# Kernel optimization log

Measured on AMD Instinct MI355X. Metric: run time of the kernel, lower is better.

The kernel has to match this reference:

```python
import jax, jax.numpy as jnp
import numpy as np

OUT_FEAT = 32  # output_feature; projected dim = OUT_FEAT**2 = 1024
D_K = OUT_FEAT ** 0.5  # NOTE: source divides by sqrt(output_feature), not sqrt(output_feature^2)


def setup_inputs() -> dict:
    key = jax.random.key(0)
    ks = jax.random.split(key, 7)
    N, D_in, D_proj = 4096, 1024, OUT_FEAT * OUT_FEAT
    s = 1.0 / np.sqrt(D_in)
    return {
        "x": jax.random.normal(ks[0], (N, D_in), jnp.float32),
        "Wq": jax.random.normal(ks[1], (D_in, D_proj), jnp.float32) * s,
        "bq": jax.random.normal(ks[2], (D_proj,), jnp.float32) * s,
        "Wk": jax.random.normal(ks[3], (D_in, D_proj), jnp.float32) * s,
        "bk": jax.random.normal(ks[4], (D_proj,), jnp.float32) * s,
        "Wv": jax.random.normal(ks[5], (D_in, D_proj), jnp.float32) * s,
        "bv": jax.random.normal(ks[6], (D_proj,), jnp.float32) * s,
    }


def reference(x, Wq, bq, Wk, bk, Wv, bv):
    # QKV projections: [N, D_proj]
    Q = x @ Wq + bq
    K = x @ Wk + bk
    V = x @ Wv + bv
    # scores: [N, N], scaled by sqrt(output_feature) per the source
    scores = (Q @ K.T) / D_K
    attn_weights = jax.nn.softmax(scores, axis=-1)
    attn_output = attn_weights @ V  # [N, D_proj]
    attn_output = attn_output.reshape(-1, OUT_FEAT, OUT_FEAT)  # mode='cov' reshape
    return attn_output, attn_weights
```

## Files before the change

kernel.cpp:

```cpp
#include <hip/hip_runtime.h>

typedef short short8 __attribute__((ext_vector_type(8)));
typedef float f32x4 __attribute__((ext_vector_type(4)));

constexpr int NROW  = 4096;
constexpr int DIN   = 1024;
constexpr int DPROJ = 1024;
constexpr float INV_DK = 0.17677669529663687f;

__device__ __forceinline__ unsigned short f2bf(float f) {
  union { float f; unsigned int u; } v; v.f = f;
  unsigned int r = v.u + 0x7FFFu + ((v.u >> 16) & 1u);
  return (unsigned short)(r >> 16);
}
__device__ __forceinline__ float bf2f(unsigned short h) {
  union { unsigned int u; float f; } v; v.u = ((unsigned int)h) << 16; return v.f;
}

template<int KB>
__device__ __forceinline__ void stage_tile(const unsigned short* __restrict__ g,
                                           long row0, long ldK, long k0,
                                           unsigned short* lds_tile, int w, int lane) {
  if constexpr (KB == 64) {
    const int rsub = lane >> 3;
    const int csw  = ((lane & 7) ^ (rsub & 7)) * 8;
#pragma unroll
    for (int it = 0; it < 4; ++it) {
      const int rowblk = w * 32 + it * 8;
      const unsigned short* src = g + (row0 + rowblk + rsub) * ldK + k0 + csw;
      unsigned short* dst = lds_tile + rowblk * 64;
      __builtin_amdgcn_global_load_lds(
          (const __attribute__((address_space(1))) unsigned int*)(const void*)src,
          (__attribute__((address_space(3))) unsigned int*)(void*)dst, 16, 0, 0);
    }
  } else {
    const int rsub = lane >> 2;
    const int csw  = ((lane & 3) ^ ((rsub >> 1) & 3)) * 8;
#pragma unroll
    for (int it = 0; it < 2; ++it) {
      const int rowblk = w * 32 + it * 16;
      const unsigned short* src = g + (row0 + rowblk + rsub) * ldK + k0 + csw;
      unsigned short* dst = lds_tile + rowblk * 32;
      __builtin_amdgcn_global_load_lds(
          (const __attribute__((address_space(1))) unsigned int*)(const void*)src,
          (__attribute__((address_space(3))) unsigned int*)(void*)dst, 16, 0, 0);
    }
  }
}

template<int SPLIT, int EPI, int KB>
__global__ __launch_bounds__(256, 2) void mfma_gemm(
    const unsigned short* __restrict__ Ah, const unsigned short* __restrict__ Al,
    const unsigned short* __restrict__ Bh, const unsigned short* __restrict__ Bl,
    const float* __restrict__ bias, float* __restrict__ Cf,
    unsigned short* __restrict__ Coh, unsigned short* __restrict__ Col,
    int M, int N, int K, float alpha)
{
  constexpr int NT = SPLIT ? 4 : 2;
  constexpr int TS = 128 * KB;
  __shared__ __align__(16) unsigned short lds[2][NT * TS];
  const int tid  = threadIdx.x;
  const int w    = tid >> 6, lane = tid & 63;
  const int wr   = w >> 1,   wc   = w & 1;
  const int lrow = lane & 15, lgrp = lane >> 4;
  const long bm = (long)blockIdx.y * 128, bn = (long)blockIdx.x * 128;

  f32x4 acc[4][4] = {};

  const int nsteps = K / KB;

  stage_tile<KB>(Ah, bm, K, 0, &lds[0][0 * TS], w, lane);
  stage_tile<KB>(Bh, bn, K, 0, &lds[0][1 * TS], w, lane);
  if constexpr (SPLIT) {
    stage_tile<KB>(Al, bm, K, 0, &lds[0][2 * TS], w, lane);
    stage_tile<KB>(Bl, bn, K, 0, &lds[0][3 * TS], w, lane);
  }

  int cur = 0;
  for (int t = 0; t < nsteps; ++t) {
    __syncthreads();
    if (t + 1 < nsteps) {
      const long k0 = (long)(t + 1) * KB;
      const int nb = cur ^ 1;
      stage_tile<KB>(Ah, bm, K, k0, &lds[nb][0 * TS], w, lane);
      stage_tile<KB>(Bh, bn, K, k0, &lds[nb][1 * TS], w, lane);
      if constexpr (SPLIT) {
        stage_tile<KB>(Al, bm, K, k0, &lds[nb][2 * TS], w, lane);
        stage_tile<KB>(Bl, bn, K, k0, &lds[nb][3 * TS], w, lane);
      }
    }
    const unsigned short* L = lds[cur];
#pragma unroll
    for (int s = 0; s < KB / 32; ++s) {
      short8 ah[4], bh[4], al[4], bl[4];
#pragma unroll
      for (int i = 0; i < 4; ++i) {
        const int ra  = wr * 64 + i * 16 + lrow;
        const int sga = (KB == 64) ? (ra & 7) : ((ra >> 1) & 3);
        const int cha = ((s * 4 + lgrp) ^ sga);
        const int offa = ra * KB + cha * 8;
        ah[i] = *(const short8*)&L[0 * TS + offa];
        if constexpr (SPLIT) al[i] = *(const short8*)&L[2 * TS + offa];
        const int rb  = wc * 64 + i * 16 + lrow;
        const int sgb = (KB == 64) ? (rb & 7) : ((rb >> 1) & 3);
        const int chb = ((s * 4 + lgrp) ^ sgb);
        const int offb = rb * KB + chb * 8;
        bh[i] = *(const short8*)&L[1 * TS + offb];
        if constexpr (SPLIT) bl[i] = *(const short8*)&L[3 * TS + offb];
      }
#pragma unroll
      for (int i = 0; i < 4; ++i)
#pragma unroll
        for (int j = 0; j < 4; ++j) {
          acc[i][j] = __builtin_amdgcn_mfma_f32_16x16x32_bf16(ah[i], bh[j], acc[i][j], 0, 0, 0);
          if constexpr (SPLIT) {
            acc[i][j] = __builtin_amdgcn_mfma_f32_16x16x32_bf16(ah[i], bl[j], acc[i][j], 0, 0, 0);
            acc[i][j] = __builtin_amdgcn_mfma_f32_16x16x32_bf16(al[i], bh[j], acc[i][j], 0, 0, 0);
          }
        }
    }
    cur ^= 1;
  }

#pragma unroll
  for (int i = 0; i < 4; ++i) {
    const long rbase = bm + wr * 64 + i * 16 + lgrp * 4;
#pragma unroll
    for (int j = 0; j < 4; ++j) {
      const long cg = bn + wc * 64 + j * 16 + lrow;
#pragma unroll
      for (int r = 0; r < 4; ++r) {
        const long rg = rbase + r;
        float v = acc[i][j][r];
        if constexpr (EPI == 0) {
          Cf[rg * N + cg] = alpha * v;
        } else if constexpr (EPI == 1) {
          v += bias[cg];
          unsigned short h = f2bf(v);
          Coh[rg * N + cg] = h;
          Col[rg * N + cg] = f2bf(v - bf2f(h));
        } else {
          v += bias[rg];
          Coh[rg * N + cg] = f2bf(v);
        }
      }
    }
  }
}

__global__ __launch_bounds__(256) void split_rows(const float* __restrict__ in,
    unsigned short* __restrict__ oh, unsigned short* __restrict__ ol, int n4)
{
  int idx = blockIdx.x * 256 + threadIdx.x;
  const int stride = gridDim.x * 256;
  for (; idx < n4; idx += stride) {
    float4 v = ((const float4*)in)[idx];
    ushort4 h, l;
    h.x = f2bf(v.x); l.x = f2bf(v.x - bf2f(h.x));
    h.y = f2bf(v.y); l.y = f2bf(v.y - bf2f(h.y));
    h.z = f2bf(v.z); l.z = f2bf(v.z - bf2f(h.z));
    h.w = f2bf(v.w); l.w = f2bf(v.w - bf2f(h.w));
    ((ushort4*)oh)[idx] = h;
    ((ushort4*)ol)[idx] = l;
  }
}

__global__ __launch_bounds__(256) void split_transpose(const float* __restrict__ W,
    unsigned short* __restrict__ oTh, unsigned short* __restrict__ oTl, int R, int C)
{
  __shared__ float t[64][65];
  const int rt = blockIdx.y * 64, ct = blockIdx.x * 64;
  const int r0 = threadIdx.x >> 4, c4 = (threadIdx.x & 15) * 4;
#pragma unroll
  for (int rr = 0; rr < 4; ++rr) {
    const int row = r0 + rr * 16;
    float4 v = *(const float4*)(W + (long)(rt + row) * C + ct + c4);
    t[row][c4 + 0] = v.x; t[row][c4 + 1] = v.y;
    t[row][c4 + 2] = v.z; t[row][c4 + 3] = v.w;
  }
  __syncthreads();
#pragma unroll
  for (int rr = 0; rr < 4; ++rr) {
    const int orow = r0 + rr * 16;
    float x0 = t[c4 + 0][orow], x1 = t[c4 + 1][orow];
    float x2 = t[c4 + 2][orow], x3 = t[c4 + 3][orow];
    ushort4 h, l;
    h.x = f2bf(x0); l.x = f2bf(x0 - bf2f(h.x));
    h.y = f2bf(x1); l.y = f2bf(x1 - bf2f(h.y));
    h.z = f2bf(x2); l.z = f2bf(x2 - bf2f(h.z));
    h.w = f2bf(x3); l.w = f2bf(x3 - bf2f(h.w));
    *(ushort4*)(oTh + (long)(ct + orow) * R + rt + c4) = h;
    *(ushort4*)(oTl + (long)(ct + orow) * R + rt + c4) = l;
  }
}

__global__ __launch_bounds__(256) void softmax_p(float* __restrict__ S,
                                                 unsigned short* __restrict__ P)
{
  const int tid = threadIdx.x;
  float* p = S + (size_t)blockIdx.x * 4096;
  unsigned short* pb = P + (size_t)blockIdx.x * 4096;
  float4 v[4];
  float mx = -3.402823466e38f;
#pragma unroll
  for (int i = 0; i < 4; ++i) {
    v[i] = *(const float4*)(p + 4 * (tid + i * 256));
    mx = fmaxf(mx, fmaxf(fmaxf(v[i].x, v[i].y), fmaxf(v[i].z, v[i].w)));
  }
#pragma unroll
  for (int off = 32; off >= 1; off >>= 1) mx = fmaxf(mx, __shfl_xor(mx, off));
  __shared__ float redm[4], reds[4];
  if ((tid & 63) == 0) redm[tid >> 6] = mx;
  __syncthreads();
  mx = fmaxf(fmaxf(redm[0], redm[1]), fmaxf(redm[2], redm[3]));

  float sum = 0.f;
#pragma unroll
  for (int i = 0; i < 4; ++i) {
    v[i].x = __expf(v[i].x - mx); v[i].y = __expf(v[i].y - mx);
    v[i].z = __expf(v[i].z - mx); v[i].w = __expf(v[i].w - mx);
    sum += (v[i].x + v[i].y) + (v[i].z + v[i].w);
  }
#pragma unroll
  for (int off = 32; off >= 1; off >>= 1) sum += __shfl_xor(sum, off);
  if ((tid & 63) == 0) reds[tid >> 6] = sum;
  __syncthreads();
  sum = (reds[0] + reds[1]) + (reds[2] + reds[3]);
  const float inv = 1.0f / sum;
#pragma unroll
  for (int i = 0; i < 4; ++i) {
    v[i].x *= inv; v[i].y *= inv; v[i].z *= inv; v[i].w *= inv;
    *(float4*)(p + 4 * (tid + i * 256)) = v[i];
    ushort4 h;
    h.x = f2bf(v[i].x); h.y = f2bf(v[i].y); h.z = f2bf(v[i].z); h.w = f2bf(v[i].w);
    *(ushort4*)(pb + 4 * (tid + i * 256)) = h;
  }
}

extern "C" void kernel_launch(void* const* d_in, const int* in_sizes, int n_in,
                              void* d_out, int out_size, void* d_ws, size_t ws_size,
                              hipStream_t stream)
{
  const float* x  = (const float*)d_in[0];
  const float* Wq = (const float*)d_in[1];
  const float* bq = (const float*)d_in[2];
  const float* Wk = (const float*)d_in[3];
  const float* bk = (const float*)d_in[4];
  const float* Wv = (const float*)d_in[5];
  const float* bv = (const float*)d_in[6];

  float* attn_out = (float*)d_out;
  float* attn_w   = attn_out + (size_t)NROW * DPROJ;

  constexpr size_t MB = 1ull << 20;
  char* sc = (char*)attn_w;
  unsigned short* xh   = (unsigned short*)(sc + 0 * MB);
  unsigned short* xl   = (unsigned short*)(sc + 8 * MB);
  unsigned short* WqTh = (unsigned short*)(sc + 16 * MB);
  unsigned short* WqTl = (unsigned short*)(sc + 18 * MB);
  unsigned short* WkTh = (unsigned short*)(sc + 20 * MB);
  unsigned short* WkTl = (unsigned short*)(sc + 22 * MB);
  unsigned short* WvTh = (unsigned short*)(sc + 24 * MB);
  unsigned short* WvTl = (unsigned short*)(sc + 26 * MB);
  char* wsb = (char*)d_ws;
  unsigned short* VT = (unsigned short*)(wsb + 0 * MB);
  unsigned short* Qh = (unsigned short*)(wsb + 8 * MB);
  unsigned short* Ql = (unsigned short*)(wsb + 16 * MB);
  unsigned short* Kh = (unsigned short*)(wsb + 24 * MB);
  unsigned short* Kl = (unsigned short*)(wsb + 32 * MB);
  unsigned short* P  = (unsigned short*)(wsb + 8 * MB);

  dim3 blk(256);

  split_rows<<<4096, blk, 0, stream>>>(x, xh, xl, NROW * DIN / 4);
  dim3 gtr(16, 16);
  split_transpose<<<gtr, blk, 0, stream>>>(Wq, WqTh, WqTl, DIN, DPROJ);
  split_transpose<<<gtr, blk, 0, stream>>>(Wk, WkTh, WkTl, DIN, DPROJ);
  split_transpose<<<gtr, blk, 0, stream>>>(Wv, WvTh, WvTl, DIN, DPROJ);

  mfma_gemm<0, 3, 64><<<dim3(NROW / 128, DPROJ / 128), blk, 0, stream>>>(
      WvTh, nullptr, xh, nullptr, bv, nullptr, VT, nullptr,
      DPROJ, NROW, DIN, 1.0f);

  mfma_gemm<1, 1, 32><<<dim3(DPROJ / 128, NROW / 128), blk, 0, stream>>>(
      xh, xl, WqTh, WqTl, bq, nullptr, Qh, Ql, NROW, DPROJ, DIN, 1.0f);
  mfma_gemm<1, 1, 32><<<dim3(DPROJ / 128, NROW / 128), blk, 0, stream>>>(
      xh, xl, WkTh, WkTl, bk, nullptr, Kh, Kl, NROW, DPROJ, DIN, 1.0f);

  mfma_gemm<1, 0, 32><<<dim3(NROW / 128, NROW / 128), blk, 0, stream>>>(
      Qh, Ql, Kh, Kl, nullptr, attn_w, nullptr, nullptr,
      NROW, NROW, DPROJ, INV_DK);

  softmax_p<<<NROW, blk, 0, stream>>>(attn_w, P);

  mfma_gemm<0, 0, 64><<<dim3(DPROJ / 128, NROW / 128), blk, 0, stream>>>(
      P, nullptr, VT, nullptr, nullptr, attn_out, nullptr, nullptr,
      NROW, DPROJ, NROW, 1.0f);
}
```

Before: 278.4 us.

## Add 256x256-tile score GEMM with direct global-to-LDS loads and phased prefetch

Replaces the 128x128 split-bf16 score GEMM (Q·K^T) with a dedicated kernel using 256x256 output tiles, 8 waves per block, and global_load_lds to stream tiles straight into LDS. The K-loop is split into four quarter phases with barriers, staggered prefetch of the next hi/lo tiles, and raised wave priority around the MFMA bursts. This aims to raise arithmetic intensity and overlap loads with compute for the largest GEMM. In exchange it uses more LDS and registers per block (128 accumulator floats per lane plus 128 KB LDS), which may reduce occupancy. The grid also drops to 256 blocks.

New measurement: 267.1 us. -4.1%, faster.

```diff
diff --git a/kernel.cpp b/kernel.cpp
--- a/kernel.cpp
+++ b/kernel.cpp
@@ -66,7 +66,6 @@
   const long bm = (long)blockIdx.y * 128, bn = (long)blockIdx.x * 128;
 
   f32x4 acc[4][4] = {};
-
   const int nsteps = K / KB;
 
   stage_tile<KB>(Ah, bm, K, 0, &lds[0][0 * TS], w, lane);
@@ -97,14 +96,12 @@
       for (int i = 0; i < 4; ++i) {
         const int ra  = wr * 64 + i * 16 + lrow;
         const int sga = (KB == 64) ? (ra & 7) : ((ra >> 1) & 3);
-        const int cha = ((s * 4 + lgrp) ^ sga);
-        const int offa = ra * KB + cha * 8;
+        const int offa = ra * KB + ((s * 4 + lgrp) ^ sga) * 8;
         ah[i] = *(const short8*)&L[0 * TS + offa];
         if constexpr (SPLIT) al[i] = *(const short8*)&L[2 * TS + offa];
         const int rb  = wc * 64 + i * 16 + lrow;
         const int sgb = (KB == 64) ? (rb & 7) : ((rb >> 1) & 3);
-        const int chb = ((s * 4 + lgrp) ^ sgb);
-        const int offb = rb * KB + chb * 8;
+        const int offb = rb * KB + ((s * 4 + lgrp) ^ sgb) * 8;
         bh[i] = *(const short8*)&L[1 * TS + offb];
         if constexpr (SPLIT) bl[i] = *(const short8*)&L[3 * TS + offb];
       }
@@ -144,6 +141,118 @@
           Coh[rg * N + cg] = f2bf(v);
         }
       }
+    }
+  }
+}
+
+__device__ __forceinline__ void stage256(const unsigned short* __restrict__ g,
+    long row0, long ldK, long k0, unsigned short* tile, int w, int lane, int rnd)
+{
+  const int row_in = rnd * 128 + w * 16 + (lane >> 2);
+  const int csw = ((lane & 3) ^ ((row_in >> 1) & 3)) * 8;
+  const unsigned short* src = g + (row0 + row_in) * ldK + k0 + csw;
+  unsigned short* dst = tile + (rnd * 128 + w * 16) * 32;
+  __builtin_amdgcn_global_load_lds(
+      (const __attribute__((address_space(1))) unsigned int*)(const void*)src,
+      (__attribute__((address_space(3))) unsigned int*)(void*)dst, 16, 0, 0);
+}
+
+__global__ __launch_bounds__(512, 2) void score_gemm256(
+    const unsigned short* __restrict__ Ah, const unsigned short* __restrict__ Al,
+    const unsigned short* __restrict__ Bh, const unsigned short* __restrict__ Bl,
+    float* __restrict__ Cf, int M, int N, int K, float alpha)
+{
+  __shared__ __align__(16) unsigned short lds[2][4 * 8192];
+  const int tid  = threadIdx.x;
+  const int w    = tid >> 6, lane = tid & 63;
+  const int wr   = w >> 2,   wc   = w & 3;
+  const int lrow = lane & 15, lgrp = lane >> 4;
+  const long bm = (long)blockIdx.y * 256, bn = (long)blockIdx.x * 256;
+
+  f32x4 acc[8][4] = {};
+  const int nsteps = K >> 5;
+
+  {
+    unsigned short* B0 = &lds[0][0];
+#pragma unroll
+    for (int r = 0; r < 2; ++r) {
+      stage256(Ah, bm, K, 0, B0 + 0 * 8192, w, lane, r);
+      stage256(Al, bm, K, 0, B0 + 1 * 8192, w, lane, r);
+      stage256(Bh, bn, K, 0, B0 + 2 * 8192, w, lane, r);
+      stage256(Bl, bn, K, 0, B0 + 3 * 8192, w, lane, r);
+    }
+  }
+  asm volatile("s_waitcnt vmcnt(0)" ::: "memory");
+
+  int cur = 0;
+  for (int t = 0; t < nsteps; ++t) {
+    const unsigned short* L = &lds[cur][0];
+    unsigned short* Ln = &lds[cur ^ 1][0];
+    const long kn = (long)(t + 1) << 5;
+    const bool pf = (t + 1 < nsteps);
+#pragma unroll
+    for (int q = 0; q < 4; ++q) {
+      __builtin_amdgcn_s_barrier();
+      __builtin_amdgcn_sched_barrier(0);
+      const int mh = q >> 1, nh = q & 1;
+      short8 a_h[4], a_l[4], b_h[2], b_l[2];
+#pragma unroll
+      for (int i = 0; i < 4; ++i) {
+        const int ra = wr * 128 + mh * 64 + i * 16 + lrow;
+        const int offa = ra * 32 + ((lgrp ^ ((ra >> 1) & 3)) * 8);
+        a_h[i] = *(const short8*)&L[0 * 8192 + offa];
+        a_l[i] = *(const short8*)&L[1 * 8192 + offa];
+      }
+#pragma unroll
+      for (int j = 0; j < 2; ++j) {
+        const int rb = wc * 64 + nh * 32 + j * 16 + lrow;
+        const int offb = rb * 32 + ((lgrp ^ ((rb >> 1) & 3)) * 8);
+        b_h[j] = *(const short8*)&L[2 * 8192 + offb];
+        b_l[j] = *(const short8*)&L[3 * 8192 + offb];
+      }
+      if (pf && q == 0) {
+#pragma unroll
+        for (int r = 0; r < 2; ++r) {
+          stage256(Ah, bm, K, kn, Ln + 0 * 8192, w, lane, r);
+          stage256(Bh, bn, K, kn, Ln + 2 * 8192, w, lane, r);
+        }
+      }
+      if (pf && q == 1) {
+#pragma unroll
+        for (int r = 0; r < 2; ++r) {
+          stage256(Al, bm, K, kn, Ln + 1 * 8192, w, lane, r);
+          stage256(Bl, bn, K, kn, Ln + 3 * 8192, w, lane, r);
+        }
+      }
+      __builtin_amdgcn_sched_barrier(0);
+      __builtin_amdgcn_s_setprio(1);
+#pragma unroll
+      for (int i = 0; i < 4; ++i)
+#pragma unroll
+        for (int j = 0; j < 2; ++j) {
+          const int ai = mh * 4 + i, aj = nh * 2 + j;
+          acc[ai][aj] = __builtin_amdgcn_mfma_f32_16x16x32_bf16(a_h[i], b_h[j], acc[ai][aj], 0, 0, 0);
+          acc[ai][aj] = __builtin_amdgcn_mfma_f32_16x16x32_bf16(a_h[i], b_l[j], acc[ai][aj], 0, 0, 0);
+          acc[ai][aj] = __builtin_amdgcn_mfma_f32_16x16x32_bf16(a_l[i], b_h[j], acc[ai][aj], 0, 0, 0);
+        }
+      __builtin_amdgcn_s_setprio(0);
+      if (q == 3) {
+        asm volatile("s_waitcnt vmcnt(0)" ::: "memory");
+        __builtin_amdgcn_sched_barrier(0);
+      }
+    }
+    cur ^= 1;
+  }
+
+#pragma unroll
+  for (int i = 0; i < 8; ++i) {
+    const long rbase = bm + wr * 128 + i * 16 + lgrp * 4;
+#pragma unroll
+    for (int j = 0; j < 4; ++j) {
+      const long cg = bn + wc * 64 + j * 16 + lrow;
+#pragma unroll
+      for (int r = 0; r < 4; ++r)
+        Cf[(rbase + r) * (long)N + cg] = alpha * acc[i][j][r];
     }
   }
 }
@@ -287,9 +396,8 @@
   mfma_gemm<1, 1, 32><<<dim3(DPROJ / 128, NROW / 128), blk, 0, stream>>>(
       xh, xl, WkTh, WkTl, bk, nullptr, Kh, Kl, NROW, DPROJ, DIN, 1.0f);
 
-  mfma_gemm<1, 0, 32><<<dim3(NROW / 128, NROW / 128), blk, 0, stream>>>(
-      Qh, Ql, Kh, Kl, nullptr, attn_w, nullptr, nullptr,
-      NROW, NROW, DPROJ, INV_DK);
+  score_gemm256<<<dim3(NROW / 256, NROW / 256), dim3(512), 0, stream>>>(
+      Qh, Ql, Kh, Kl, attn_w, NROW, NROW, DPROJ, INV_DK);
 
   softmax_p<<<NROW, blk, 0, stream>>>(attn_w, P);
 
```
